# Performance work log

Hardware: AMD Instinct MI355X
Metric: run time of the kernel (lower is better)

The kernel has to match this reference:

```python
import jax, jax.numpy as jnp
import numpy as np

N = 10000
E = 320000
IN_DIM = 128
HID = 64


def setup_inputs() -> dict:
    key = jax.random.key(0)
    k1, k2, k3, k4 = jax.random.split(key, 4)
    x = jax.random.normal(k1, (N, IN_DIM), dtype=jnp.float32)
    edge_index = jax.random.randint(k2, (2, E), 0, N, dtype=jnp.int64)
    # Glorot-style init for GCN linear weights
    W1 = jax.random.normal(k3, (IN_DIM, HID), dtype=jnp.float32) * (1.0 / np.sqrt(IN_DIM))
    b1 = jnp.zeros((HID,), dtype=jnp.float32)
    W2 = jax.random.normal(k4, (HID, HID), dtype=jnp.float32) * (1.0 / np.sqrt(HID))
    b2 = jnp.zeros((HID,), dtype=jnp.float32)
    return {"x": x, "edge_index": edge_index, "W1": W1, "b1": b1, "W2": W2, "b2": b2}


def gcn_conv(x, src, dst, W, b, n_nodes):
    # PyG GCNConv: add self-loops, symmetric normalization D^-1/2 (A+I) D^-1/2, XW + b
    xw = x @ W                                           # [N, H]
    deg = jax.ops.segment_sum(jnp.ones_like(dst, dtype=x.dtype), dst,
                              num_segments=n_nodes)      # [N]
    deg_inv_sqrt = jnp.where(deg > 0, jax.lax.rsqrt(deg), 0.0)
    norm = deg_inv_sqrt[src] * deg_inv_sqrt[dst]         # [E+N]
    msg = xw[src] * norm[:, None]                        # gather + scale
    out = jax.ops.segment_sum(msg, dst, num_segments=n_nodes)  # scatter-add
    return out + b


def reference(x, edge_index, W1, b1, W2, b2):
    n_nodes = x.shape[0]
    loops = jnp.arange(n_nodes, dtype=edge_index.dtype)
    src = jnp.concatenate([edge_index[0], loops])
    dst = jnp.concatenate([edge_index[1], loops])
    h = jax.nn.relu(gcn_conv(x, src, dst, W1, b1, n_nodes))
    h = gcn_conv(h, src, dst, W2, b2, n_nodes)
    prob_adj = jax.nn.sigmoid(h @ h.T)                   # [N, N] dense
    return prob_adj
```

## Files before the change

kernel.cpp:

```cpp
#include <hip/hip_runtime.h>
#include <hip/hip_bf16.h>

#define NN 10000
#define INDIM 128
#define HID 64
#define CB 1250
#define GB 2500
#define SB 1250
#define PB 313

typedef __attribute__((ext_vector_type(8))) short bf16x8;
typedef __attribute__((ext_vector_type(4))) float f32x4;

__global__ __launch_bounds__(256) void k_count_gemm1(
    const int* __restrict__ dst, int E, int* __restrict__ cnt,
    const float* __restrict__ x, const float* __restrict__ W1,
    float* __restrict__ xw) {
  __shared__ float w[INDIM * HID];
  int b = blockIdx.x, t = threadIdx.x;
  if (b < CB) {
    int e = b * 256 + t;
    if (e < E) atomicAdd(&cnt[dst[e]], 1);
  } else {
    for (int i = t; i < INDIM * HID; i += 256) w[i] = W1[i];
    __syncthreads();
    int r = (b - CB) * 4 + (t >> 6);
    int j = t & 63;
    float2 xv = ((const float2*)(x + (size_t)r * INDIM))[j & (INDIM / 2 - 1)];
    float acc = 0.f;
    #pragma unroll
    for (int k = 0; k < INDIM; k++) {
      float xk = __shfl((k & 1) ? xv.y : xv.x, k >> 1, 64);
      acc = fmaf(xk, w[k * HID + j], acc);
    }
    xw[(size_t)r * HID + j] = acc;
  }
}

__global__ __launch_bounds__(1024) void k_scan(const int* __restrict__ cnt, int E,
                                               int* __restrict__ off, int* __restrict__ cursor,
                                               float* __restrict__ dis) {
  __shared__ int wsum[16];
  int t = threadIdx.x, lane = t & 63, wid = t >> 6;
  const int CH = (NN + 1023) / 1024;
  int base = t * CH;
  int s = 0;
  #pragma unroll
  for (int i = 0; i < CH; i++) { int idx = base + i; if (idx < NN) s += cnt[idx]; }
  int xs = s;
  #pragma unroll
  for (int d = 1; d < 64; d <<= 1) {
    int v = __shfl_up(xs, d, 64);
    if (lane >= d) xs += v;
  }
  if (lane == 63) wsum[wid] = xs;
  __syncthreads();
  if (wid == 0) {
    int w = (lane < 16) ? wsum[lane] : 0;
    #pragma unroll
    for (int d = 1; d < 16; d <<= 1) {
      int v = __shfl_up(w, d, 64);
      if (lane >= d) w += v;
    }
    if (lane < 16) wsum[lane] = w;
  }
  __syncthreads();
  int run = ((wid > 0) ? wsum[wid - 1] : 0) + (xs - s);
  #pragma unroll
  for (int i = 0; i < CH; i++) {
    int idx = base + i;
    if (idx < NN) {
      off[idx] = run;
      cursor[idx] = run;
      int c = cnt[idx];
      dis[idx] = rsqrtf((float)(c + 1));
      run += c;
    }
  }
  if (t == 0) off[NN] = E;
}

__global__ __launch_bounds__(256) void k_scatter_scale(
    const int* __restrict__ src, const int* __restrict__ dst, int E,
    int* __restrict__ cursor, int* __restrict__ csr,
    const float* __restrict__ dis, float* __restrict__ xw) {
  int b = blockIdx.x, t = threadIdx.x;
  if (b < SB) {
    int e = b * 256 + t;
    if (e < E) {
      int p = atomicAdd(&cursor[dst[e]], 1);
      csr[p] = src[e];
    }
  } else {
    size_t i8 = ((size_t)(b - SB) * 256 + t) * 8;
    if (i8 < (size_t)NN * HID) {
      float ds = dis[i8 >> 6];
      float4* p0 = (float4*)(xw + i8);
      float4 v0 = p0[0], v1 = p0[1];
      v0.x *= ds; v0.y *= ds; v0.z *= ds; v0.w *= ds;
      v1.x *= ds; v1.y *= ds; v1.z *= ds; v1.w *= ds;
      p0[0] = v0; p0[1] = v1;
    }
  }
}

__global__ __launch_bounds__(256) void k_agg1_gemm2(
    const float* __restrict__ xw, const int* __restrict__ off,
    const int* __restrict__ csr, const float* __restrict__ dis,
    const float* __restrict__ b1, const float* __restrict__ W2,
    float* __restrict__ hB) {
  __shared__ float w[HID * HID];
  int t = threadIdx.x;
  for (int i = t; i < HID * HID; i += 256) w[i] = W2[i];
  __syncthreads();
  int wid = t >> 6, lane = t & 63;
  int d = blockIdx.x * 4 + wid;
  int s0 = off[d], s1 = off[d + 1];
  float acc = xw[(size_t)d * HID + lane];
  int k = s0;
  for (; k + 8 <= s1; k += 8) {
    int i0 = csr[k],     i1 = csr[k + 1], i2 = csr[k + 2], i3 = csr[k + 3];
    int i4 = csr[k + 4], i5 = csr[k + 5], i6 = csr[k + 6], i7 = csr[k + 7];
    float v0 = xw[(size_t)i0 * HID + lane], v1 = xw[(size_t)i1 * HID + lane];
    float v2 = xw[(size_t)i2 * HID + lane], v3 = xw[(size_t)i3 * HID + lane];
    float v4 = xw[(size_t)i4 * HID + lane], v5 = xw[(size_t)i5 * HID + lane];
    float v6 = xw[(size_t)i6 * HID + lane], v7 = xw[(size_t)i7 * HID + lane];
    acc += ((v0 + v1) + (v2 + v3)) + ((v4 + v5) + (v6 + v7));
  }
  for (; k < s1; k++) acc += xw[(size_t)csr[k] * HID + lane];
  float h = fmaxf(acc * dis[d] + b1[lane], 0.f);
  float acc2 = 0.f;
  #pragma unroll
  for (int kk = 0; kk < HID; kk++)
    acc2 = fmaf(__shfl(h, kk, 64), w[kk * HID + lane], acc2);
  hB[(size_t)d * HID + lane] = acc2 * dis[d];
}

__global__ __launch_bounds__(256) void k_agg2(
    const float* __restrict__ hB, const int* __restrict__ off,
    const int* __restrict__ csr, const float* __restrict__ dis,
    const float* __restrict__ b2, __hip_bfloat16* __restrict__ h2b) {
  int t = threadIdx.x, wid = t >> 6, lane = t & 63;
  int d = blockIdx.x * 4 + wid;
  int s0 = off[d], s1 = off[d + 1];
  float acc = hB[(size_t)d * HID + lane];
  int k = s0;
  for (; k + 8 <= s1; k += 8) {
    int i0 = csr[k],     i1 = csr[k + 1], i2 = csr[k + 2], i3 = csr[k + 3];
    int i4 = csr[k + 4], i5 = csr[k + 5], i6 = csr[k + 6], i7 = csr[k + 7];
    float v0 = hB[(size_t)i0 * HID + lane], v1 = hB[(size_t)i1 * HID + lane];
    float v2 = hB[(size_t)i2 * HID + lane], v3 = hB[(size_t)i3 * HID + lane];
    float v4 = hB[(size_t)i4 * HID + lane], v5 = hB[(size_t)i5 * HID + lane];
    float v6 = hB[(size_t)i6 * HID + lane], v7 = hB[(size_t)i7 * HID + lane];
    acc += ((v0 + v1) + (v2 + v3)) + ((v4 + v5) + (v6 + v7));
  }
  for (; k < s1; k++) acc += hB[(size_t)csr[k] * HID + lane];
  float v = acc * dis[d] + b2[lane];
  h2b[(size_t)d * HID + lane] = __float2bfloat16(v);
}

__global__ __launch_bounds__(256) void k_final(const short* __restrict__ hb,
                                               float* __restrict__ out) {
  const int T = (NN + 63) / 64;
  int wid = threadIdx.x >> 6, lane = threadIdx.x & 63;
  int tx = blockIdx.x * 2 + (wid & 1);
  int ty = blockIdx.y * 2 + (wid >> 1);
  if (tx >= T || ty >= T) return;
  int rowbase = tx * 64, colbase = ty * 64;
  int m = lane & 15, q = lane >> 4;

  bf16x8 a0[4], a1[4], b0[4], b1[4];
  #pragma unroll
  for (int rt = 0; rt < 4; rt++) {
    int r = rowbase + rt * 16 + m; r = r < NN ? r : NN - 1;
    const bf16x8* p = reinterpret_cast<const bf16x8*>(hb + (size_t)r * HID + q * 8);
    a0[rt] = p[0]; a1[rt] = p[4];
  }
  #pragma unroll
  for (int ct = 0; ct < 4; ct++) {
    int r = colbase + ct * 16 + m; r = r < NN ? r : NN - 1;
    const bf16x8* p = reinterpret_cast<const bf16x8*>(hb + (size_t)r * HID + q * 8);
    b0[ct] = p[0]; b1[ct] = p[4];
  }

  f32x4 acc[4][4];
  #pragma unroll
  for (int rt = 0; rt < 4; rt++)
    #pragma unroll
    for (int ct = 0; ct < 4; ct++) {
      f32x4 z = {0.f, 0.f, 0.f, 0.f};
      z = __builtin_amdgcn_mfma_f32_16x16x32_bf16(a0[rt], b0[ct], z, 0, 0, 0);
      z = __builtin_amdgcn_mfma_f32_16x16x32_bf16(a1[rt], b1[ct], z, 0, 0, 0);
      acc[rt][ct] = z;
    }

  #pragma unroll
  for (int ct = 0; ct < 4; ct++)
    #pragma unroll
    for (int rt = 0; rt < 4; rt++) {
      if (rowbase + rt * 16 < NN && colbase + ct * 16 < NN) {
        f32x4 z = acc[rt][ct], o;
        #pragma unroll
        for (int r = 0; r < 4; r++)
          o[r] = __builtin_amdgcn_rcpf(1.0f + __expf(-z[r]));
        size_t orow = (size_t)(colbase + ct * 16 + m);
        size_t ocol = (size_t)(rowbase + rt * 16 + q * 4);
        *reinterpret_cast<f32x4*>(out + orow * NN + ocol) = o;
      }
    }
}

extern "C" void kernel_launch(void* const* d_in, const int* in_sizes, int n_in,
                              void* d_out, int out_size, void* d_ws, size_t ws_size,
                              hipStream_t stream) {
  const float* x  = (const float*)d_in[0];
  const int*   ei = (const int*)d_in[1];
  const float* W1 = (const float*)d_in[2];
  const float* b1 = (const float*)d_in[3];
  const float* W2 = (const float*)d_in[4];
  const float* b2 = (const float*)d_in[5];
  int E = in_sizes[1] / 2;
  const int* src = ei;
  const int* dst = ei + E;

  char* base = (char*)d_out;
  float* xwA  = (float*)(base);
  float* hB   = (float*)(base + 2560000);
  int*   csr  = (int*)(base + 5120000);
  char*  p2   = base + 5120000 + 4 * (size_t)E;
  int*   cnt    = (int*)(p2);
  int*   off    = (int*)(p2 + 40064);
  int*   cursor = (int*)(p2 + 80128);
  float* dis    = (float*)(p2 + 120192);
  __hip_bfloat16* h2b = (__hip_bfloat16*)d_ws;

  hipMemsetAsync(cnt, 0, NN * sizeof(int), stream);
  k_count_gemm1<<<CB + GB, 256, 0, stream>>>(dst, E, cnt, x, W1, xwA);
  k_scan<<<1, 1024, 0, stream>>>(cnt, E, off, cursor, dis);
  k_scatter_scale<<<SB + PB, 256, 0, stream>>>(src, dst, E, cursor, csr,
                                               dis, xwA);
  k_agg1_gemm2<<<NN / 4, 256, 0, stream>>>(xwA, off, csr, dis, b1, W2, hB);
  k_agg2<<<NN / 4, 256, 0, stream>>>(hB, off, csr, dis, b2, h2b);

  const int T = (NN + 63) / 64;
  dim3 gf((T + 1) / 2, (T + 1) / 2);
  k_final<<<gf, 256, 0, stream>>>((const short*)h2b, (float*)d_out);
}
```

Baseline: 201.1 us.

## Retile final sigmoid(HH^T) kernel to 16-row output strips per block

Result: slower. 245.3 us (+22.0%).

```diff
diff --git a/kernel.cpp b/kernel.cpp
--- a/kernel.cpp
+++ b/kernel.cpp
@@ -161,53 +161,45 @@
 
 __global__ __launch_bounds__(256) void k_final(const short* __restrict__ hb,
                                                float* __restrict__ out) {
-  const int T = (NN + 63) / 64;
   int wid = threadIdx.x >> 6, lane = threadIdx.x & 63;
-  int tx = blockIdx.x * 2 + (wid & 1);
-  int ty = blockIdx.y * 2 + (wid >> 1);
-  if (tx >= T || ty >= T) return;
-  int rowbase = tx * 64, colbase = ty * 64;
   int m = lane & 15, q = lane >> 4;
-
-  bf16x8 a0[4], a1[4], b0[4], b1[4];
-  #pragma unroll
-  for (int rt = 0; rt < 4; rt++) {
-    int r = rowbase + rt * 16 + m; r = r < NN ? r : NN - 1;
+  int abase = blockIdx.x * 512 + wid * 128;
+  int bbase = blockIdx.y * 16;
+
+  bf16x8 b0, b1;
+  {
+    const bf16x8* p = reinterpret_cast<const bf16x8*>(hb + (size_t)(bbase + m) * HID + q * 8);
+    b0 = p[0]; b1 = p[4];
+  }
+  bf16x8 a0[8], a1[8];
+  #pragma unroll
+  for (int rt = 0; rt < 8; rt++) {
+    int r = abase + rt * 16 + m; r = r < NN ? r : NN - 1;
     const bf16x8* p = reinterpret_cast<const bf16x8*>(hb + (size_t)r * HID + q * 8);
     a0[rt] = p[0]; a1[rt] = p[4];
   }
-  #pragma unroll
-  for (int ct = 0; ct < 4; ct++) {
-    int r = colbase + ct * 16 + m; r = r < NN ? r : NN - 1;
-    const bf16x8* p = reinterpret_cast<const bf16x8*>(hb + (size_t)r * HID + q * 8);
-    b0[ct] = p[0]; b1[ct] = p[4];
-  }
-
-  f32x4 acc[4][4];
-  #pragma unroll
-  for (int rt = 0; rt < 4; rt++)
-    #pragma unroll
-    for (int ct = 0; ct < 4; ct++) {
-      f32x4 z = {0.f, 0.f, 0.f, 0.f};
-      z = __builtin_amdgcn_mfma_f32_16x16x32_bf16(a0[rt], b0[ct], z, 0, 0, 0);
-      z = __builtin_amdgcn_mfma_f32_16x16x32_bf16(a1[rt], b1[ct], z, 0, 0, 0);
-      acc[rt][ct] = z;
-    }
-
-  #pragma unroll
-  for (int ct = 0; ct < 4; ct++)
-    #pragma unroll
-    for (int rt = 0; rt < 4; rt++) {
-      if (rowbase + rt * 16 < NN && colbase + ct * 16 < NN) {
-        f32x4 z = acc[rt][ct], o;
-        #pragma unroll
-        for (int r = 0; r < 4; r++)
-          o[r] = __builtin_amdgcn_rcpf(1.0f + __expf(-z[r]));
-        size_t orow = (size_t)(colbase + ct * 16 + m);
-        size_t ocol = (size_t)(rowbase + rt * 16 + q * 4);
-        *reinterpret_cast<f32x4*>(out + orow * NN + ocol) = o;
-      }
-    }
+
+  f32x4 acc[8];
+  #pragma unroll
+  for (int rt = 0; rt < 8; rt++) {
+    f32x4 z = {0.f, 0.f, 0.f, 0.f};
+    z = __builtin_amdgcn_mfma_f32_16x16x32_bf16(a0[rt], b0, z, 0, 0, 0);
+    z = __builtin_amdgcn_mfma_f32_16x16x32_bf16(a1[rt], b1, z, 0, 0, 0);
+    acc[rt] = z;
+  }
+
+  #pragma unroll
+  for (int rt = 0; rt < 8; rt++) {
+    if (abase + rt * 16 < NN) {
+      f32x4 z = acc[rt], o;
+      #pragma unroll
+      for (int j = 0; j < 4; j++)
+        o[j] = __builtin_amdgcn_rcpf(1.0f + __expf(-z[j]));
+      size_t orow = (size_t)(bbase + m);
+      size_t ocol = (size_t)(abase + rt * 16 + q * 4);
+      *reinterpret_cast<f32x4*>(out + orow * NN + ocol) = o;
+    }
+  }
 }
 
 extern "C" void kernel_launch(void* const* d_in, const int* in_sizes, int n_in,
@@ -242,7 +234,6 @@
   k_agg1_gemm2<<<NN / 4, 256, 0, stream>>>(xwA, off, csr, dis, b1, W2, hB);
   k_agg2<<<NN / 4, 256, 0, stream>>>(hB, off, csr, dis, b2, h2b);
 
-  const int T = (NN + 63) / 64;
-  dim3 gf((T + 1) / 2, (T + 1) / 2);
+  dim3 gf((NN + 511) / 512, NN / 16);
   k_final<<<gf, 256, 0, stream>>>((const short*)h2b, (float*)d_out);
 }
```
